# Optimization experiments

Hardware: AMD Instinct MI355X
Metric: run time of the kernel (lower is better)

Reference implementation:

```python
import jax, jax.numpy as jnp
import numpy as np

OUT_H, OUT_W = 6, 6
SPATIAL_SCALE = 1.0
SAMPLING_RATIO = 2  # fixed grid (Mask R-CNN standard); aligned=True semantics below


def setup_inputs() -> dict:
    key = jax.random.key(0)
    k1, k2, k3 = jax.random.split(key, 3)
    B, C, H, W = 8, 256, 128, 128
    N = 64
    x = jax.random.normal(k1, (B, C, H, W), dtype=jnp.float32)
    # boxes in (x1, y1, x2, y2) image coords, guaranteed x1<x2, y1<y2
    xs = jnp.sort(jax.random.uniform(k2, (B, N, 2), dtype=jnp.float32) * W, axis=-1)
    ys = jnp.sort(jax.random.uniform(k3, (B, N, 2), dtype=jnp.float32) * H, axis=-1)
    boxes = jnp.stack([xs[..., 0], ys[..., 0], xs[..., 1], ys[..., 1]], axis=-1)
    return {"x": x, "boxes": boxes}


def _interp_1d(coords, size):
    # torchvision bilinear_interpolate semantics along one axis
    valid = (coords >= -1.0) & (coords <= size)
    c = jnp.maximum(coords, 0.0)
    low0 = jnp.floor(c).astype(jnp.int32)
    at_edge = low0 >= size - 1
    low = jnp.where(at_edge, size - 1, low0)
    high = jnp.where(at_edge, size - 1, low0 + 1)
    frac = jnp.where(at_edge, 0.0, c - low0.astype(c.dtype))
    w_lo = jnp.where(valid, 1.0 - frac, 0.0)
    w_hi = jnp.where(valid, frac, 0.0)
    return low, high, w_lo, w_hi


def _roi_align_one(feat, boxes):
    # feat: [C, H, W], boxes: [N, 4] -> [N, C, OUT_H, OUT_W]
    C, H, W = feat.shape
    gh, gw = SAMPLING_RATIO, SAMPLING_RATIO
    x1 = boxes[:, 0] * SPATIAL_SCALE - 0.5  # aligned=True half-pixel offset
    y1 = boxes[:, 1] * SPATIAL_SCALE - 0.5
    x2 = boxes[:, 2] * SPATIAL_SCALE - 0.5
    y2 = boxes[:, 3] * SPATIAL_SCALE - 0.5
    bin_h = (y2 - y1) / OUT_H  # [N]
    bin_w = (x2 - x1) / OUT_W
    # sample positions in bin units: pos[k] for k = bin_idx*g + i -> bin_idx + (i+0.5)/g
    pos_y = (jnp.arange(OUT_H, dtype=jnp.float32)[:, None]
             + (jnp.arange(gh, dtype=jnp.float32)[None, :] + 0.5) / gh).reshape(-1)
    pos_x = (jnp.arange(OUT_W, dtype=jnp.float32)[:, None]
             + (jnp.arange(gw, dtype=jnp.float32)[None, :] + 0.5) / gw).reshape(-1)
    ys = y1[:, None] + pos_y[None, :] * bin_h[:, None]  # [N, OUT_H*gh]
    xs = x1[:, None] + pos_x[None, :] * bin_w[:, None]  # [N, OUT_W*gw]
    yl, yh, wy0, wy1 = _interp_1d(ys, H)
    xl, xh, wx0, wx1 = _interp_1d(xs, W)
    flat = feat.reshape(C, H * W)

    def g(yi, xi):
        idx = yi[:, :, None] * W + xi[:, None, :]  # [N, Yg, Xg]
        return flat[:, idx]                        # [C, N, Yg, Xg]

    val = (wy0[:, :, None] * wx0[:, None, :] * g(yl, xl)
           + wy0[:, :, None] * wx1[:, None, :] * g(yl, xh)
           + wy1[:, :, None] * wx0[:, None, :] * g(yh, xl)
           + wy1[:, :, None] * wx1[:, None, :] * g(yh, xh))
    N = boxes.shape[0]
    # average the gh*gw samples within each output bin (count = gh*gw)
    val = val.reshape(C, N, OUT_H, gh, OUT_W, gw).mean(axis=(3, 5))
    return jnp.transpose(val, (1, 0, 2, 3))  # [N, C, OUT_H, OUT_W]


def reference(x, boxes):
    # x: [B, C, H, W], boxes: [B, N, 4] -> [B, N, C, OUT_H, OUT_W]
    return jax.vmap(_roi_align_one)(x, boxes)
```

## Files before the change

kernel.cpp:

```cpp
#include <hip/hip_runtime.h>

#define B 8
#define C 256
#define H 128
#define W 128
#define HW (H * W)
#define NBOX 64
#define OUT_H 6
#define OUT_W 6
#define NBINS (OUT_H * OUT_W)
#define ENT_PER_BOX 24
#define TBL_N (B * NBOX * ENT_PER_BOX)
#define PITCH 132
#define NOUT (NBOX * NBINS)

__device__ __forceinline__ void interp1d(float coord, int size,
                                         int& lo, float& w0, float& w1) {
    bool valid = (coord >= -1.0f) && (coord <= (float)size);
    float c = fmaxf(coord, 0.0f);
    int low0 = (int)floorf(c);
    bool at_edge = (low0 >= size - 1);
    lo = at_edge ? (size - 1) : low0;
    float frac = at_edge ? 0.0f : (c - (float)low0);
    w0 = valid ? (1.0f - frac) : 0.0f;
    w1 = valid ? frac : 0.0f;
}

__global__ __launch_bounds__(256)
void table_kernel(const float* __restrict__ boxes, float4* __restrict__ tbl) {
    const int idx = blockIdx.x * 256 + threadIdx.x;
    if (idx >= TBL_N) return;
    const int bn = idx / ENT_PER_BOX;
    const int k = idx - bn * ENT_PER_BOX;
    const float* bx = boxes + bn * 4;
    const float x1 = bx[0] - 0.5f;
    const float y1 = bx[1] - 0.5f;
    const float x2 = bx[2] - 0.5f;
    const float y2 = bx[3] - 0.5f;
    const int kk = (k < 12) ? k : (k - 12);
    const float pos = (float)(kk >> 1) + ((float)(kk & 1) + 0.5f) * 0.5f;
    float coord;
    if (k < 12) coord = y1 + pos * ((y2 - y1) * (1.0f / OUT_H));
    else        coord = x1 + pos * ((x2 - x1) * (1.0f / OUT_W));
    int lo; float w0, w1;
    interp1d(coord, 128, lo, w0, w1);
    tbl[idx] = make_float4(w0, w1, (float)lo, 0.0f);
}

__global__ __launch_bounds__(1024, 8)
void roi_plane_kernel(const float* __restrict__ x,
                      const float4* __restrict__ tbl,
                      float* __restrict__ out) {
    __shared__ float plane[(H + 1) * PITCH];
    const int bid = blockIdx.x;
    const int b = bid >> 8;
    const int c = bid & 255;
    const int tid = threadIdx.x;

    const float4* src = (const float4*)(x + (size_t)bid * HW);
    #pragma unroll
    for (int i = 0; i < 4; ++i) {
        const int m = i * 1024 + tid;
        const int row = m >> 5;
        const int col = (m & 31) << 2;
        *(float4*)&plane[row * PITCH + col] = src[m];
    }
    const float4 z4 = make_float4(0.f, 0.f, 0.f, 0.f);
    if (tid < H) *(float4*)&plane[tid * PITCH + W] = z4;
    else if (tid >= 1024 - PITCH / 4)
        *(float4*)&plane[H * PITCH + (tid - (1024 - PITCH / 4)) * 4] = z4;
    __syncthreads();

    const float4* tb = tbl + b * (NBOX * ENT_PER_BOX);
    float* ob = out + ((size_t)b * NBOX * C + c) * NBINS;

    #pragma unroll 1
    for (int it = 0; it < 3; ++it) {
        const int k = it * 1024 + tid;
        if (k < NOUT) {
            const int n = k / NBINS;
            const int bin = k - n * NBINS;
            const int oh = bin / OUT_W;
            const int ow = bin - oh * OUT_W;
            const int e = n * ENT_PER_BOX;

            const float4 tx0 = tb[e + 12 + ow * 2 + 0];
            const float4 tx1 = tb[e + 12 + ow * 2 + 1];
            const int xl0 = (int)tx0.z, xl1 = (int)tx1.z;

            float acc = 0.0f;
            #pragma unroll
            for (int i = 0; i < 2; ++i) {
                const float4 ty = tb[e + oh * 2 + i];
                const int yl = (int)ty.z;
                const float* r0 = plane + yl * PITCH;
                const float* r1 = r0 + PITCH;
                acc += ty.x * (tx0.x * r0[xl0] + tx0.y * r0[xl0 + 1])
                     + ty.y * (tx0.x * r1[xl0] + tx0.y * r1[xl0 + 1]);
                acc += ty.x * (tx1.x * r0[xl1] + tx1.y * r0[xl1 + 1])
                     + ty.y * (tx1.x * r1[xl1] + tx1.y * r1[xl1 + 1]);
            }
            ob[(size_t)n * (C * NBINS) + bin] = acc * 0.25f;
        }
    }
}

__global__ __launch_bounds__(256)
void roi_align_nchw_kernel(const float* __restrict__ x,
                           const float* __restrict__ boxes,
                           float* __restrict__ out) {
    const int bn = blockIdx.x;
    const int b = bn / NBOX;
    const int c = threadIdx.x;

    __shared__ int   s_yl[12], s_xl[12];
    __shared__ float s_wy0[12], s_wy1[12], s_wx0[12], s_wx1[12];

    const float* bx = boxes + (bn * 4);
    const float x1 = bx[0] - 0.5f, y1 = bx[1] - 0.5f;
    const float x2 = bx[2] - 0.5f, y2 = bx[3] - 0.5f;
    const float bin_h = (y2 - y1) * (1.0f / OUT_H);
    const float bin_w = (x2 - x1) * (1.0f / OUT_W);

    if (threadIdx.x < 12) {
        int k = threadIdx.x;
        float pos = (float)(k >> 1) + ((float)(k & 1) + 0.5f) * 0.5f;
        interp1d(y1 + pos * bin_h, H, s_yl[k], s_wy0[k], s_wy1[k]);
    } else if (threadIdx.x < 24) {
        int k = threadIdx.x - 12;
        float pos = (float)(k >> 1) + ((float)(k & 1) + 0.5f) * 0.5f;
        interp1d(x1 + pos * bin_w, W, s_xl[k], s_wx0[k], s_wx1[k]);
    }
    __syncthreads();

    const float* feat = x + ((size_t)(b * C + c) * HW);
    float* op = out + ((size_t)(bn * C + c) * NBINS);

    for (int oh = 0; oh < OUT_H; ++oh) {
        for (int ow = 0; ow < OUT_W; ++ow) {
            float v = 0.0f;
            for (int i = 0; i < 2; ++i) {
                const int sy = oh * 2 + i;
                const int yl = s_yl[sy], yh = min(yl + 1, H - 1);
                const float wy0 = s_wy0[sy], wy1 = s_wy1[sy];
                for (int j = 0; j < 2; ++j) {
                    const int sx = ow * 2 + j;
                    const int xl = s_xl[sx], xh = min(xl + 1, W - 1);
                    v += wy0 * (s_wx0[sx] * feat[yl * W + xl] + s_wx1[sx] * feat[yl * W + xh])
                       + wy1 * (s_wx0[sx] * feat[yh * W + xl] + s_wx1[sx] * feat[yh * W + xh]);
                }
            }
            op[oh * OUT_W + ow] = v * 0.25f;
        }
    }
}

extern "C" void kernel_launch(void* const* d_in, const int* in_sizes, int n_in,
                              void* d_out, int out_size, void* d_ws, size_t ws_size,
                              hipStream_t stream) {
    const float* x     = (const float*)d_in[0];
    const float* boxes = (const float*)d_in[1];
    float* out = (float*)d_out;

    const size_t tbl_bytes = (size_t)TBL_N * sizeof(float4);
    if (ws_size >= tbl_bytes) {
        float4* tbl = (float4*)d_ws;
        table_kernel<<<(TBL_N + 255) / 256, 256, 0, stream>>>(boxes, tbl);
        roi_plane_kernel<<<B * C, 1024, 0, stream>>>(x, tbl, out);
    } else {
        roi_align_nchw_kernel<<<B * NBOX, C, 0, stream>>>(x, boxes, out);
    }
}
```

Baseline: 201.0 us.

## Fuse table build into persistent multi-plane kernel with double-buffered LDS prefetch

Removes the separate table kernel and instead has each block compute its batch's interpolation table in shared memory. Each block then processes 8 channel planes, prefetching the next plane into registers while computing the current one, and writes it into a second LDS buffer. This is meant to remove one launch, avoid re-reading the table from global memory, and overlap global loads with LDS gather compute. In exchange, LDS use per block rises to about 160KB, which allows only one block per CU, and the grid shrinks to 256 blocks, which may under-fill the GPU.

```diff
diff --git a/kernel.cpp b/kernel.cpp
--- a/kernel.cpp
+++ b/kernel.cpp
@@ -10,9 +10,12 @@
 #define OUT_W 6
 #define NBINS (OUT_H * OUT_W)
 #define ENT_PER_BOX 24
-#define TBL_N (B * NBOX * ENT_PER_BOX)
+#define TBL_PER_B (NBOX * ENT_PER_BOX)
 #define PITCH 132
+#define PLANE_ELEMS ((H + 1) * PITCH)
 #define NOUT (NBOX * NBINS)
+#define PLANES_PER_BLOCK 8
+#define NBLK (B * C / PLANES_PER_BLOCK)
 
 __device__ __forceinline__ void interp1d(float coord, int size,
                                          int& lo, float& w0, float& w1) {
@@ -26,132 +29,123 @@
     w1 = valid ? frac : 0.0f;
 }
 
-__global__ __launch_bounds__(256)
-void table_kernel(const float* __restrict__ boxes, float4* __restrict__ tbl) {
-    const int idx = blockIdx.x * 256 + threadIdx.x;
-    if (idx >= TBL_N) return;
-    const int bn = idx / ENT_PER_BOX;
-    const int k = idx - bn * ENT_PER_BOX;
-    const float* bx = boxes + bn * 4;
-    const float x1 = bx[0] - 0.5f;
-    const float y1 = bx[1] - 0.5f;
-    const float x2 = bx[2] - 0.5f;
-    const float y2 = bx[3] - 0.5f;
-    const int kk = (k < 12) ? k : (k - 12);
-    const float pos = (float)(kk >> 1) + ((float)(kk & 1) + 0.5f) * 0.5f;
-    float coord;
-    if (k < 12) coord = y1 + pos * ((y2 - y1) * (1.0f / OUT_H));
-    else        coord = x1 + pos * ((x2 - x1) * (1.0f / OUT_W));
-    int lo; float w0, w1;
-    interp1d(coord, 128, lo, w0, w1);
-    tbl[idx] = make_float4(w0, w1, (float)lo, 0.0f);
-}
+__global__ __launch_bounds__(1024, 4)
+void roi_persist_kernel(const float* __restrict__ x,
+                        const float* __restrict__ boxes,
+                        float* __restrict__ out) {
+    __shared__ float buf0[PLANE_ELEMS];
+    __shared__ float buf1[PLANE_ELEMS];
+    __shared__ float4 stab[TBL_PER_B];
 
-__global__ __launch_bounds__(1024, 8)
-void roi_plane_kernel(const float* __restrict__ x,
-                      const float4* __restrict__ tbl,
-                      float* __restrict__ out) {
-    __shared__ float plane[(H + 1) * PITCH];
-    const int bid = blockIdx.x;
-    const int b = bid >> 8;
-    const int c = bid & 255;
+    const int blk = blockIdx.x;
+    const int b = blk >> 5;
+    const int c0 = (blk & 31) * PLANES_PER_BLOCK;
     const int tid = threadIdx.x;
 
-    const float4* src = (const float4*)(x + (size_t)bid * HW);
     #pragma unroll
-    for (int i = 0; i < 4; ++i) {
-        const int m = i * 1024 + tid;
-        const int row = m >> 5;
-        const int col = (m & 31) << 2;
-        *(float4*)&plane[row * PITCH + col] = src[m];
+    for (int i = tid; i < TBL_PER_B; i += 1024) {
+        const int n = i / ENT_PER_BOX;
+        const int k = i - n * ENT_PER_BOX;
+        const float* bx = boxes + ((size_t)(b * NBOX + n)) * 4;
+        const float x1 = bx[0] - 0.5f;
+        const float y1 = bx[1] - 0.5f;
+        const float x2 = bx[2] - 0.5f;
+        const float y2 = bx[3] - 0.5f;
+        const int kk = (k < 12) ? k : (k - 12);
+        const float pos = (float)(kk >> 1) + ((float)(kk & 1) + 0.5f) * 0.5f;
+        float coord;
+        if (k < 12) coord = y1 + pos * ((y2 - y1) * (1.0f / OUT_H));
+        else        coord = x1 + pos * ((x2 - x1) * (1.0f / OUT_W));
+        int lo; float w0, w1;
+        interp1d(coord, 128, lo, w0, w1);
+        stab[i] = make_float4(w0, w1, (float)lo, 0.0f);
     }
+
     const float4 z4 = make_float4(0.f, 0.f, 0.f, 0.f);
-    if (tid < H) *(float4*)&plane[tid * PITCH + W] = z4;
-    else if (tid >= 1024 - PITCH / 4)
-        *(float4*)&plane[H * PITCH + (tid - (1024 - PITCH / 4)) * 4] = z4;
-    __syncthreads();
+    if (tid < H) {
+        *(float4*)&buf0[tid * PITCH + W] = z4;
+        *(float4*)&buf1[tid * PITCH + W] = z4;
+    } else if (tid >= 1024 - PITCH / 4) {
+        const int j = (tid - (1024 - PITCH / 4)) * 4;
+        *(float4*)&buf0[H * PITCH + j] = z4;
+        *(float4*)&buf1[H * PITCH + j] = z4;
+    }
 
-    const float4* tb = tbl + b * (NBOX * ENT_PER_BOX);
-    float* ob = out + ((size_t)b * NBOX * C + c) * NBINS;
-
-    #pragma unroll 1
-    for (int it = 0; it < 3; ++it) {
-        const int k = it * 1024 + tid;
-        if (k < NOUT) {
-            const int n = k / NBINS;
-            const int bin = k - n * NBINS;
-            const int oh = bin / OUT_W;
-            const int ow = bin - oh * OUT_W;
-            const int e = n * ENT_PER_BOX;
-
-            const float4 tx0 = tb[e + 12 + ow * 2 + 0];
-            const float4 tx1 = tb[e + 12 + ow * 2 + 1];
-            const int xl0 = (int)tx0.z, xl1 = (int)tx1.z;
-
-            float acc = 0.0f;
-            #pragma unroll
-            for (int i = 0; i < 2; ++i) {
-                const float4 ty = tb[e + oh * 2 + i];
-                const int yl = (int)ty.z;
-                const float* r0 = plane + yl * PITCH;
-                const float* r1 = r0 + PITCH;
-                acc += ty.x * (tx0.x * r0[xl0] + tx0.y * r0[xl0 + 1])
-                     + ty.y * (tx0.x * r1[xl0] + tx0.y * r1[xl0 + 1]);
-                acc += ty.x * (tx1.x * r0[xl1] + tx1.y * r0[xl1 + 1])
-                     + ty.y * (tx1.x * r1[xl1] + tx1.y * r1[xl1 + 1]);
-            }
-            ob[(size_t)n * (C * NBINS) + bin] = acc * 0.25f;
+    {
+        const float4* src = (const float4*)(x + (size_t)(b * C + c0) * HW);
+        float4 r0 = src[tid];
+        float4 r1 = src[1024 + tid];
+        float4 r2 = src[2048 + tid];
+        float4 r3 = src[3072 + tid];
+        #pragma unroll
+        for (int i = 0; i < 4; ++i) {
+            const int m = i * 1024 + tid;
+            const float4 v = (i == 0) ? r0 : (i == 1) ? r1 : (i == 2) ? r2 : r3;
+            *(float4*)&buf0[(m >> 5) * PITCH + ((m & 31) << 2)] = v;
         }
-    }
-}
-
-__global__ __launch_bounds__(256)
-void roi_align_nchw_kernel(const float* __restrict__ x,
-                           const float* __restrict__ boxes,
-                           float* __restrict__ out) {
-    const int bn = blockIdx.x;
-    const int b = bn / NBOX;
-    const int c = threadIdx.x;
-
-    __shared__ int   s_yl[12], s_xl[12];
-    __shared__ float s_wy0[12], s_wy1[12], s_wx0[12], s_wx1[12];
-
-    const float* bx = boxes + (bn * 4);
-    const float x1 = bx[0] - 0.5f, y1 = bx[1] - 0.5f;
-    const float x2 = bx[2] - 0.5f, y2 = bx[3] - 0.5f;
-    const float bin_h = (y2 - y1) * (1.0f / OUT_H);
-    const float bin_w = (x2 - x1) * (1.0f / OUT_W);
-
-    if (threadIdx.x < 12) {
-        int k = threadIdx.x;
-        float pos = (float)(k >> 1) + ((float)(k & 1) + 0.5f) * 0.5f;
-        interp1d(y1 + pos * bin_h, H, s_yl[k], s_wy0[k], s_wy1[k]);
-    } else if (threadIdx.x < 24) {
-        int k = threadIdx.x - 12;
-        float pos = (float)(k >> 1) + ((float)(k & 1) + 0.5f) * 0.5f;
-        interp1d(x1 + pos * bin_w, W, s_xl[k], s_wx0[k], s_wx1[k]);
     }
     __syncthreads();
 
-    const float* feat = x + ((size_t)(b * C + c) * HW);
-    float* op = out + ((size_t)(bn * C + c) * NBINS);
+    float* cur = buf0;
+    float* nxt = buf1;
 
-    for (int oh = 0; oh < OUT_H; ++oh) {
-        for (int ow = 0; ow < OUT_W; ++ow) {
-            float v = 0.0f;
-            for (int i = 0; i < 2; ++i) {
-                const int sy = oh * 2 + i;
-                const int yl = s_yl[sy], yh = min(yl + 1, H - 1);
-                const float wy0 = s_wy0[sy], wy1 = s_wy1[sy];
-                for (int j = 0; j < 2; ++j) {
-                    const int sx = ow * 2 + j;
-                    const int xl = s_xl[sx], xh = min(xl + 1, W - 1);
-                    v += wy0 * (s_wx0[sx] * feat[yl * W + xl] + s_wx1[sx] * feat[yl * W + xh])
-                       + wy1 * (s_wx0[sx] * feat[yh * W + xl] + s_wx1[sx] * feat[yh * W + xh]);
-                }
+    #pragma unroll 1
+    for (int p = 0; p < PLANES_PER_BLOCK; ++p) {
+        float4 r0, r1, r2, r3;
+        if (p < PLANES_PER_BLOCK - 1) {
+            const float4* src = (const float4*)(x + (size_t)(b * C + c0 + p + 1) * HW);
+            r0 = src[tid];
+            r1 = src[1024 + tid];
+            r2 = src[2048 + tid];
+            r3 = src[3072 + tid];
+        }
+
+        const int c = c0 + p;
+        float* ob = out + ((size_t)(b * NBOX) * C + c) * NBINS;
+        #pragma unroll 1
+        for (int it = 0; it < 3; ++it) {
+            const int k = it * 1024 + tid;
+            if (k < NOUT) {
+                const int n = k / NBINS;
+                const int bin = k - n * NBINS;
+                const int oh = bin / OUT_W;
+                const int ow = bin - oh * OUT_W;
+                const float4* e = stab + n * ENT_PER_BOX;
+
+                const float4 ty0 = e[oh * 2 + 0];
+                const float4 ty1 = e[oh * 2 + 1];
+                const float4 tx0 = e[12 + ow * 2 + 0];
+                const float4 tx1 = e[12 + ow * 2 + 1];
+                const int xl0 = (int)tx0.z, xl1 = (int)tx1.z;
+
+                const float* a0 = cur + (int)ty0.z * PITCH;
+                const float* a1 = a0 + PITCH;
+                float acc = ty0.x * (tx0.x * a0[xl0] + tx0.y * a0[xl0 + 1])
+                          + ty0.y * (tx0.x * a1[xl0] + tx0.y * a1[xl0 + 1])
+                          + ty0.x * (tx1.x * a0[xl1] + tx1.y * a0[xl1 + 1])
+                          + ty0.y * (tx1.x * a1[xl1] + tx1.y * a1[xl1 + 1]);
+
+                const float* q0 = cur + (int)ty1.z * PITCH;
+                const float* q1 = q0 + PITCH;
+                acc += ty1.x * (tx0.x * q0[xl0] + tx0.y * q0[xl0 + 1])
+                     + ty1.y * (tx0.x * q1[xl0] + tx0.y * q1[xl0 + 1])
+                     + ty1.x * (tx1.x * q0[xl1] + tx1.y * q0[xl1 + 1])
+                     + ty1.y * (tx1.x * q1[xl1] + tx1.y * q1[xl1 + 1]);
+
+                ob[(size_t)n * (C * NBINS) + bin] = acc * 0.25f;
             }
-            op[oh * OUT_W + ow] = v * 0.25f;
         }
+        __syncthreads();
+        if (p < PLANES_PER_BLOCK - 1) {
+            #pragma unroll
+            for (int i = 0; i < 4; ++i) {
+                const int m = i * 1024 + tid;
+                const float4 v = (i == 0) ? r0 : (i == 1) ? r1 : (i == 2) ? r2 : r3;
+                *(float4*)&nxt[(m >> 5) * PITCH + ((m & 31) << 2)] = v;
+            }
+        }
+        __syncthreads();
+        float* t = cur; cur = nxt; nxt = t;
     }
 }
 
@@ -162,12 +156,5 @@
     const float* boxes = (const float*)d_in[1];
     float* out = (float*)d_out;
 
-    const size_t tbl_bytes = (size_t)TBL_N * sizeof(float4);
-    if (ws_size >= tbl_bytes) {
-        float4* tbl = (float4*)d_ws;
-        table_kernel<<<(TBL_N + 255) / 256, 256, 0, stream>>>(boxes, tbl);
-        roi_plane_kernel<<<B * C, 1024, 0, stream>>>(x, tbl, out);
-    } else {
-        roi_align_nchw_kernel<<<B * NBOX, C, 0, stream>>>(x, boxes, out);
-    }
+    roi_persist_kernel<<<NBLK, 1024, 0, stream>>>(x, boxes, out);
 }
```

Result: no change. 200.5 us (-0.2%).
